# Optimization experiments

Measured on AMD Instinct MI355X. Metric: run time of the kernel, lower is better.

Reference implementation:

```python
import jax, jax.numpy as jnp
import numpy as np

N, DEG = 20000, 16
E = N * DEG
D_IN, D_HID, D_OUT, L = 1024, 512, 128, 3


def setup_inputs() -> dict:
    key = jax.random.key(0)
    ks = jax.random.split(key, 16)
    scale = 0.02
    X = jax.random.normal(ks[0], (N, D_IN), dtype=jnp.float32)
    senders = jax.random.randint(ks[1], (E,), 0, N)
    receivers = jnp.repeat(jnp.arange(N), DEG)  # sorted, every node has DEG neighbors
    inp = {"X": X, "senders": senders, "receivers": receivers}
    ki = 2
    for l in range(L):
        din = D_IN >> l
        dh = D_HID >> l
        inp[f"lw{l}"] = jax.random.normal(ks[ki], (2 * din, dh), jnp.float32) * scale; ki += 1
        inp[f"lb{l}"] = jnp.zeros((dh,), jnp.float32)
        inp[f"aw{l}"] = jax.random.normal(ks[ki], (din, dh), jnp.float32) * scale; ki += 1
        inp[f"aq{l}"] = jax.random.normal(ks[ki], (dh,), jnp.float32) * scale; ki += 1
    inp["ow"] = jax.random.normal(ks[ki], (D_HID >> (L - 1), D_OUT), jnp.float32) * scale
    inp["ob"] = jnp.zeros((D_OUT,), jnp.float32)
    return inp


def _attend(h, senders, receivers, aw, aq):
    # scores depend only on the neighbor (sender) embedding: q @ relu(W h_j)
    logits = jnp.einsum('nh,h->n', jax.nn.relu(h @ aw), aq)            # [N]
    el = logits[senders]                                               # [E]
    m = jax.ops.segment_max(el, receivers, num_segments=N)            # per-receiver max
    w = jnp.exp(el - m[receivers])                                     # [E]
    denom = jax.ops.segment_sum(w, receivers, num_segments=N)         # [N]
    msg = jax.ops.segment_sum(w[:, None] * h[senders], receivers, num_segments=N)  # [N,D]
    return msg / denom[:, None]


def reference(X, senders, receivers,
              lw0, lb0, aw0, aq0,
              lw1, lb1, aw1, aq1,
              lw2, lb2, aw2, aq2,
              ow, ob):
    params = [(lw0, lb0, aw0, aq0), (lw1, lb1, aw1, aq1), (lw2, lb2, aw2, aq2)]
    h = X
    for lw, lb, aw, aq in params:
        hN = _attend(h, senders, receivers, aw, aq)
        h = jax.nn.relu(jnp.concatenate([h, hN], axis=1) @ lw + lb)
    return h[14] @ ow + ob
```

## Files before the change

### kernel.cpp

```cpp
#include <hip/hip_runtime.h>
#include <math.h>

typedef unsigned short ushort_t;
typedef __attribute__((ext_vector_type(8))) short short8;
typedef __attribute__((ext_vector_type(4))) float f32x4;

#define NN    20000
#define DEG   16
constexpr int MAXL2 = 1 + DEG;
constexpr int MAXL1 = MAXL2 + MAXL2*DEG;
constexpr int MAXL0 = MAXL1*DEG;
constexpr int L0PAD = 73 * 64;
constexpr int NWBLK = 512;

__device__ __forceinline__ ushort_t f2bf(float f) {
    unsigned u = __float_as_uint(f);
    return (ushort_t)((u + 0x7FFFu + ((u >> 16) & 1u)) >> 16);
}

__global__ __launch_bounds__(256)
void k_frontier(const int* __restrict__ senders,
                int* list2, int* inv2, int* list1, int* inv1,
                int* list0, int* inv0, int* list3, int* cnts, float4* zp, int n4) {
    int t = threadIdx.x;
    if (blockIdx.x > 0) {
        int i = (blockIdx.x - 1) * 256 + t;
        if (i < n4) zp[i] = make_float4(0.f, 0.f, 0.f, 0.f);
        return;
    }
    __shared__ unsigned bm[625];
    __shared__ int cnt;
    auto clear = [&]() { for (int i = t; i < 625; i += 256) bm[i] = 0u; if (t == 0) cnt = 0; };
    auto tryadd = [&](int node, int* list, int* inv) {
        unsigned bit = 1u << (node & 31);
        unsigned old = atomicOr(&bm[node >> 5], bit);
        if (!(old & bit)) { int p = atomicAdd(&cnt, 1); list[p] = node; inv[node] = p; }
    };
    clear(); __syncthreads();
    if (t < 17) { int node = (t < 16) ? senders[14 * DEG + t] : 14; tryadd(node, list2, inv2); }
    __syncthreads();
    int c2 = cnt; if (t == 0) cnts[2] = c2;
    __syncthreads(); clear(); __syncthreads();
    for (int i = t; i < c2 * 17; i += 256) {
        int r = i / 17, k = i - 17 * r;
        int node = (k < 16) ? senders[list2[r] * DEG + k] : list2[r];
        tryadd(node, list1, inv1);
    }
    __syncthreads();
    int c1 = cnt; if (t == 0) cnts[1] = c1;
    __syncthreads(); clear(); __syncthreads();
    for (int i = t; i < c1 * 16; i += 256) {
        int r = i >> 4, k = i & 15;
        tryadd(senders[list1[r] * DEG + k], list0, inv0);
    }
    __syncthreads();
    if (t == 0) { cnts[0] = cnt; cnts[3] = 1; list3[0] = 14; }
}

__global__ __launch_bounds__(256)
void k_prep(const float* __restrict__ W, ushort_t* __restrict__ WT,
            const float* __restrict__ X, const int* __restrict__ list0,
            const int* __restrict__ cnt0, ushort_t* __restrict__ Xg) {
    int t = threadIdx.x;
    if (blockIdx.x < NWBLK) {
        __shared__ float tile[32][33];
        int b = blockIdx.x;
        int bx = b & 15, by = b >> 4;
        int i0 = t >> 3, j0 = (t & 7) * 4;
        int k = by * 32 + i0, n0 = bx * 32;
        float4 v = *(const float4*)(W + (size_t)k * 512 + n0 + j0);
        tile[i0][j0] = v.x; tile[i0][j0 + 1] = v.y; tile[i0][j0 + 2] = v.z; tile[i0][j0 + 3] = v.w;
        __syncthreads();
        int n = n0 + i0, kc = j0;
        ushort_t* p = WT + (size_t)n * 1024 + by * 32 + kc;
        p[0] = f2bf(tile[kc][i0]); p[1] = f2bf(tile[kc + 1][i0]);
        p[2] = f2bf(tile[kc + 2][i0]); p[3] = f2bf(tile[kc + 3][i0]);
    } else {
        int r = blockIdx.x - NWBLK;
        int rc = *cnt0;
        ushort_t o0 = 0, o1 = 0, o2 = 0, o3 = 0;
        if (r < rc) {
            float4 v = *(const float4*)(X + (size_t)list0[r] * 1024 + t * 4);
            o0 = f2bf(v.x); o1 = f2bf(v.y); o2 = f2bf(v.z); o3 = f2bf(v.w);
        }
        ushort_t* p = Xg + (size_t)r * 1024 + t * 4;
        p[0] = o0; p[1] = o1; p[2] = o2; p[3] = o3;
    }
}

__global__ __launch_bounds__(256)
void k_logits_mfma(const ushort_t* __restrict__ Xg,
                   const ushort_t* __restrict__ WT,
                   const float* __restrict__ aq, float* __restrict__ lgc,
                   const int* __restrict__ cnt, int K) {
    __shared__ short As[64 * 40];
    __shared__ short Bs[64 * 40];
    int rcnt = *cnt;
    int row0 = blockIdx.x * 64;
    if (row0 >= rcnt) return;
    int col0 = blockIdx.y * 64;
    int t = threadIdx.x;
    int w = t >> 6, lane = t & 63;

    int sr = t >> 2, sk = (t & 3) * 8;
    const ushort_t* ap = Xg + (size_t)(row0 + sr) * K + sk;
    const ushort_t* bp = WT + (size_t)(col0 + sr) * K + sk;

    int fm = lane & 15, fq = lane >> 4;
    const short* arow = As + (w * 16 + fm) * 40 + fq * 8;
    const short* brow = Bs + fm * 40 + fq * 8;

    f32x4 acc0 = {0.f,0.f,0.f,0.f}, acc1 = {0.f,0.f,0.f,0.f};
    f32x4 acc2 = {0.f,0.f,0.f,0.f}, acc3 = {0.f,0.f,0.f,0.f};

    short8 pa = *(const short8*)(ap);
    short8 pb = *(const short8*)(bp);
    for (int k0 = 0; k0 < K; k0 += 32) {
        *(short8*)(As + sr * 40 + sk) = pa;
        *(short8*)(Bs + sr * 40 + sk) = pb;
        __syncthreads();
        if (k0 + 32 < K) {
            pa = *(const short8*)(ap + k0 + 32);
            pb = *(const short8*)(bp + k0 + 32);
        }
        short8 af = *(const short8*)arow;
        short8 b0 = *(const short8*)(brow);
        short8 b1 = *(const short8*)(brow + 16 * 40);
        short8 b2 = *(const short8*)(brow + 32 * 40);
        short8 b3 = *(const short8*)(brow + 48 * 40);
        acc0 = __builtin_amdgcn_mfma_f32_16x16x32_bf16(af, b0, acc0, 0, 0, 0);
        acc1 = __builtin_amdgcn_mfma_f32_16x16x32_bf16(af, b1, acc1, 0, 0, 0);
        acc2 = __builtin_amdgcn_mfma_f32_16x16x32_bf16(af, b2, acc2, 0, 0, 0);
        acc3 = __builtin_amdgcn_mfma_f32_16x16x32_bf16(af, b3, acc3, 0, 0, 0);
        __syncthreads();
    }

    float aqv0 = aq[col0 + fm], aqv1 = aq[col0 + 16 + fm];
    float aqv2 = aq[col0 + 32 + fm], aqv3 = aq[col0 + 48 + fm];
#pragma unroll
    for (int r = 0; r < 4; r++) {
        float v = fmaxf(acc0[r], 0.f) * aqv0 + fmaxf(acc1[r], 0.f) * aqv1
                + fmaxf(acc2[r], 0.f) * aqv2 + fmaxf(acc3[r], 0.f) * aqv3;
#pragma unroll
        for (int off = 1; off < 16; off <<= 1) v += __shfl_xor(v, off);
        if (fm == 0) atomicAdd(&lgc[row0 + w * 16 + fq * 4 + r], v);
    }
}

__global__ __launch_bounds__(256)
void k_matmul(const float* __restrict__ A1, const float* __restrict__ A2,
              const int* __restrict__ list, const int* __restrict__ inv,
              const float* __restrict__ B, const float* __restrict__ aq,
              float* __restrict__ C, const int* __restrict__ cnt,
              int amode, int omode, int K1, int K2, int NC, int KS) {
    __shared__ float As[32][68];
    __shared__ float Bs[32][64];
    __shared__ float rowsum[64];

    int rcnt = *cnt;
    int row0 = blockIdx.x * 64;
    if (row0 >= rcnt) return;
    int col0 = blockIdx.y * 64;
    int K = K1 + K2;
    int kbeg = blockIdx.z * KS;
    int kend = kbeg + KS; if (kend > K) kend = K;

    int t = threadIdx.x;
    int ty = t >> 4, tx = t & 15;
    int lr = t >> 2, kaoff = (t & 3) * 4;
    int grow = row0 + lr;
    bool rowValid = grow < rcnt;
    const float* rp1 = A1;
    const float* rp2 = A2;
    if (rowValid) {
        int hrow;
        if (amode == 0) hrow = grow;
        else { int node = list[grow]; hrow = (amode == 2) ? inv[node] : node; }
        rp1 = A1 + (size_t)hrow * K1;
        rp2 = A2 + (size_t)grow * K2;
    }
    const float* Bp = B + col0;
    int bidx0 = t, bidx1 = t + 256;

    auto loadA = [&](int k) -> float4 {
        if (!rowValid) return make_float4(0.f, 0.f, 0.f, 0.f);
        const float* src = (k < K1) ? (rp1 + k) : (rp2 + (k - K1));
        return *(const float4*)src;
    };
    auto loadB = [&](int idx, int k0) -> float4 {
        int row = idx >> 4, c4 = (idx & 15) * 4;
        return *(const float4*)(Bp + (size_t)(k0 + row) * NC + c4);
    };

    float4 pa0 = loadA(kbeg + kaoff);
    float4 pa1 = loadA(kbeg + kaoff + 16);
    float4 pb0 = loadB(bidx0, kbeg);
    float4 pb1 = loadB(bidx1, kbeg);

    float acc[4][4] = {};
    for (int k0 = kbeg; k0 < kend; k0 += 32) {
        As[kaoff + 0][lr] = pa0.x; As[kaoff + 1][lr] = pa0.y;
        As[kaoff + 2][lr] = pa0.z; As[kaoff + 3][lr] = pa0.w;
        As[kaoff + 16][lr] = pa1.x; As[kaoff + 17][lr] = pa1.y;
        As[kaoff + 18][lr] = pa1.z; As[kaoff + 19][lr] = pa1.w;
        *(float4*)&Bs[bidx0 >> 4][(bidx0 & 15) * 4] = pb0;
        *(float4*)&Bs[bidx1 >> 4][(bidx1 & 15) * 4] = pb1;
        __syncthreads();
        if (k0 + 32 < kend) {
            pa0 = loadA(k0 + 32 + kaoff);
            pa1 = loadA(k0 + 32 + kaoff + 16);
            pb0 = loadB(bidx0, k0 + 32);
            pb1 = loadB(bidx1, k0 + 32);
        }
#pragma unroll
        for (int kk = 0; kk < 32; kk++) {
            float4 a4 = *(const float4*)&As[kk][ty * 4];
            float4 b4 = *(const float4*)&Bs[kk][tx * 4];
            float a[4] = {a4.x, a4.y, a4.z, a4.w};
            float b[4] = {b4.x, b4.y, b4.z, b4.w};
#pragma unroll
            for (int i = 0; i < 4; i++)
#pragma unroll
                for (int j = 0; j < 4; j++) acc[i][j] += a[i] * b[j];
        }
        __syncthreads();
    }

    if (omode == 0) {
#pragma unroll
        for (int i = 0; i < 4; i++) {
            int r = row0 + ty * 4 + i;
            if (r < rcnt) {
                float* Crow = C + (size_t)r * NC + col0 + tx * 4;
#pragma unroll
                for (int j = 0; j < 4; j++) atomicAdd(&Crow[j], acc[i][j]);
            }
        }
    } else {
        if (t < 64) rowsum[t] = 0.f;
        __syncthreads();
        float aqv[4];
#pragma unroll
        for (int j = 0; j < 4; j++) aqv[j] = aq[col0 + tx * 4 + j];
#pragma unroll
        for (int i = 0; i < 4; i++) {
            float s = 0.f;
#pragma unroll
            for (int j = 0; j < 4; j++) {
                float v = acc[i][j];
                v = v > 0.f ? v : 0.f;
                s += v * aqv[j];
            }
            atomicAdd(&rowsum[ty * 4 + i], s);
        }
        __syncthreads();
        if (t < 64) {
            int r = row0 + t;
            if (r < rcnt) atomicAdd(&C[r], rowsum[t]);
        }
    }
}

__global__ void k_bias_relu(const float* __restrict__ C, const float* __restrict__ b,
                            float* __restrict__ H, const int* __restrict__ cnt, int ncShift) {
    int rcnt = *cnt;
    int NC = 1 << ncShift;
    int e = blockIdx.x * 256 + threadIdx.x;
    int r = e >> ncShift;
    if (r >= rcnt) return;
    int c = e & (NC - 1);
    float v = C[(size_t)r * NC + c] + b[c];
    H[(size_t)r * NC + c] = v > 0.f ? v : 0.f;
}

__global__ __launch_bounds__(256)
void k_agg(const float* __restrict__ Hsrc, const int* __restrict__ invH,
           const float* __restrict__ lgc, const int* __restrict__ invL,
           const int* __restrict__ senders,
           const int* __restrict__ listN, const int* __restrict__ cntN,
           float* __restrict__ hN, int din) {
    __shared__ int   s_row[DEG];
    __shared__ float s_w[DEG];
    __shared__ float s_scale;
    int b = blockIdx.x;
    if (b >= *cntN) return;
    int n = listN[b];
    int t = threadIdx.x;
    if (t < DEG) {
        int s = senders[n * DEG + t];
        s_row[t] = invH ? invH[s] : s;
        s_w[t] = lgc[invL ? invL[s] : s];
    }
    __syncthreads();
    if (t == 0) {
        float m = -1e30f;
        for (int k = 0; k < DEG; k++) m = fmaxf(m, s_w[k]);
        float d = 0.f;
        for (int k = 0; k < DEG; k++) { float w = expf(s_w[k] - m); s_w[k] = w; d += w; }
        s_scale = 1.f / d;
    }
    __syncthreads();
    float scale = s_scale;
    for (int dI = t; dI < din; dI += 256) {
        float acc = 0.f;
#pragma unroll
        for (int k = 0; k < DEG; k++)
            acc += s_w[k] * Hsrc[(size_t)s_row[k] * din + dI];
        hN[(size_t)b * din + dI] = acc * scale;
    }
}

__global__ __launch_bounds__(512)
void k_out(const float* __restrict__ C2, const float* __restrict__ lb2,
           const float* __restrict__ OW, const float* __restrict__ OB,
           float* __restrict__ out) {
    __shared__ float h3s[128];
    __shared__ float part[4][128];
    int t = threadIdx.x;
    if (t < 128) { float v = C2[t] + lb2[t]; h3s[t] = v > 0.f ? v : 0.f; }
    __syncthreads();
    int j = t & 127, s = t >> 7;
    float a = 0.f;
    for (int k = s * 32; k < s * 32 + 32; k++) a += h3s[k] * OW[(size_t)k * 128 + j];
    part[s][j] = a;
    __syncthreads();
    if (t < 128) out[t] = OB[t] + part[0][t] + part[1][t] + part[2][t] + part[3][t];
}

extern "C" void kernel_launch(void* const* d_in, const int* in_sizes, int n_in,
                              void* d_out, int out_size, void* d_ws, size_t ws_size,
                              hipStream_t stream) {
    const float* X       = (const float*)d_in[0];
    const int*   senders = (const int*)d_in[1];
    const float* lw0 = (const float*)d_in[3];
    const float* lb0 = (const float*)d_in[4];
    const float* aw0 = (const float*)d_in[5];
    const float* aq0 = (const float*)d_in[6];
    const float* lw1 = (const float*)d_in[7];
    const float* lb1 = (const float*)d_in[8];
    const float* aw1 = (const float*)d_in[9];
    const float* aq1 = (const float*)d_in[10];
    const float* lw2 = (const float*)d_in[11];
    const float* lb2 = (const float*)d_in[12];
    const float* aw2 = (const float*)d_in[13];
    const float* aq2 = (const float*)d_in[14];
    const float* owp = (const float*)d_in[15];
    const float* obp = (const float*)d_in[16];
    float* out = (float*)d_out;

    char* ws = (char*)d_ws;
    size_t off = 0;
    auto alloc = [&](size_t nbytes) -> void* {
        void* p = ws + off;
        off += (nbytes + 255) & ~(size_t)255;
        return p;
    };
    float* lgc0 = (float*)alloc(L0PAD * 4);
    float* lgc1 = (float*)alloc(MAXL1 * 4);
    float* lgc2 = (float*)alloc(MAXL2 * 4);
    float* C0   = (float*)alloc((size_t)MAXL1 * 512 * 4);
    float* C1   = (float*)alloc((size_t)MAXL2 * 256 * 4);
    float* C2   = (float*)alloc(128 * 4);
    size_t zero_end = off;
    int* inv0  = (int*)alloc(NN * 4);
    int* inv1  = (int*)alloc(NN * 4);
    int* inv2  = (int*)alloc(NN * 4);
    int* list0 = (int*)alloc(L0PAD * 4);
    int* list1 = (int*)alloc(MAXL1 * 4);
    int* list2 = (int*)alloc(MAXL2 * 4);
    int* list3 = (int*)alloc(4);
    int* cnts  = (int*)alloc(4 * 4);
    ushort_t* Xg  = (ushort_t*)alloc((size_t)L0PAD * 1024 * 2);
    ushort_t* awT = (ushort_t*)alloc((size_t)512 * 1024 * 2);
    float* hN0c = (float*)alloc((size_t)MAXL1 * 1024 * 4);
    float* h1c  = (float*)alloc((size_t)MAXL1 * 512 * 4);
    float* hN1c = (float*)alloc((size_t)MAXL2 * 512 * 4);
    float* h2c  = (float*)alloc((size_t)MAXL2 * 256 * 4);
    float* hN2c = (float*)alloc(256 * 4);
    (void)in_sizes; (void)n_in; (void)out_size; (void)ws_size;

    int nz4 = (int)(zero_end / 16);
    int nzb = (nz4 + 255) / 256;

    hipLaunchKernelGGL(k_frontier, dim3(1 + nzb), dim3(256), 0, stream,
                       senders, list2, inv2, list1, inv1, list0, inv0, list3, cnts,
                       (float4*)ws, nz4);
    hipLaunchKernelGGL(k_prep, dim3(NWBLK + L0PAD), dim3(256), 0, stream,
                       aw0, awT, X, list0, cnts + 0, Xg);

    hipLaunchKernelGGL(k_logits_mfma, dim3(73, 512 / 64, 1), dim3(256), 0, stream,
                       Xg, awT, aq0, lgc0, cnts + 0, 1024);
    hipLaunchKernelGGL(k_agg, dim3(MAXL1), dim3(256), 0, stream,
                       X, (const int*)nullptr, lgc0, inv0, senders, list1, cnts + 1, hN0c, 1024);
    hipLaunchKernelGGL(k_matmul, dim3((MAXL1 + 63) / 64, 512 / 64, 8), dim3(256), 0, stream,
                       X, hN0c, list1, (int*)nullptr, lw0, aq0, C0, cnts + 1,
                       1, 0, 1024, 1024, 512, 256);
    hipLaunchKernelGGL(k_bias_relu, dim3((MAXL1 * 512 + 255) / 256), dim3(256), 0, stream,
                       C0, lb0, h1c, cnts + 1, 9);

    hipLaunchKernelGGL(k_matmul, dim3((MAXL1 + 63) / 64, 256 / 64, 1), dim3(256), 0, stream,
                       h1c, h1c, list1, (int*)nullptr, aw1, aq1, lgc1, cnts + 1,
                       0, 1, 512, 0, 256, 512);
    hipLaunchKernelGGL(k_agg, dim3(MAXL2), dim3(256), 0, stream,
                       h1c, inv1, lgc1, inv1, senders, list2, cnts + 2, hN1c, 512);
    hipLaunchKernelGGL(k_matmul, dim3(1, 256 / 64, 8), dim3(256), 0, stream,
                       h1c, hN1c, list2, inv1, lw1, aq1, C1, cnts + 2,
                       2, 0, 512, 512, 256, 128);
    hipLaunchKernelGGL(k_bias_relu, dim3((MAXL2 * 256 + 255) / 256), dim3(256), 0, stream,
                       C1, lb1, h2c, cnts + 2, 8);

    hipLaunchKernelGGL(k_matmul, dim3(1, 128 / 64, 1), dim3(256), 0, stream,
                       h2c, h2c, list2, (int*)nullptr, aw2, aq2, lgc2, cnts + 2,
                       0, 1, 256, 0, 128, 256);
    hipLaunchKernelGGL(k_agg, dim3(1), dim3(256), 0, stream,
                       h2c, inv2, lgc2, inv2, senders, list3, cnts + 3, hN2c, 256);
    hipLaunchKernelGGL(k_matmul, dim3(1, 128 / 64, 4), dim3(256), 0, stream,
                       h2c, hN2c, list3, inv2, lw2, aq2, C2, cnts + 3,
                       2, 0, 256, 256, 128, 128);
    hipLaunchKernelGGL(k_out, dim3(1), dim3(512), 0, stream, C2, lb2, owp, obp, out);
}
```

Baseline: 284.1 us.

## Fuse all GNN stages into one persistent kernel with grid-wide barriers

Replaces roughly a dozen separate kernel launches with a single persistent kernel of 256 blocks. The stages are separated by software grid barriers built on global atomic counters. It also drops the level-0 frontier dedup: each edge's sender row is gathered straight into the bf16 staging buffer, and attention logits are indexed per edge. The workspace is zeroed with a memset instead of extra zeroing blocks. This removes launch overhead and inter-kernel gaps, but adds spin-barrier cost and relies on all 256 blocks being co-resident. It also computes duplicate logits for repeated senders.

```diff
diff --git a/kernel.cpp b/kernel.cpp
--- a/kernel.cpp
+++ b/kernel.cpp
@@ -9,163 +9,34 @@
 #define DEG   16
 constexpr int MAXL2 = 1 + DEG;
 constexpr int MAXL1 = MAXL2 + MAXL2*DEG;
-constexpr int MAXL0 = MAXL1*DEG;
 constexpr int L0PAD = 73 * 64;
-constexpr int NWBLK = 512;
+constexpr int GRID  = 256;
 
 __device__ __forceinline__ ushort_t f2bf(float f) {
     unsigned u = __float_as_uint(f);
     return (ushort_t)((u + 0x7FFFu + ((u >> 16) & 1u)) >> 16);
 }
-
-__global__ __launch_bounds__(256)
-void k_frontier(const int* __restrict__ senders,
-                int* list2, int* inv2, int* list1, int* inv1,
-                int* list0, int* inv0, int* list3, int* cnts, float4* zp, int n4) {
-    int t = threadIdx.x;
-    if (blockIdx.x > 0) {
-        int i = (blockIdx.x - 1) * 256 + t;
-        if (i < n4) zp[i] = make_float4(0.f, 0.f, 0.f, 0.f);
-        return;
-    }
-    __shared__ unsigned bm[625];
-    __shared__ int cnt;
-    auto clear = [&]() { for (int i = t; i < 625; i += 256) bm[i] = 0u; if (t == 0) cnt = 0; };
-    auto tryadd = [&](int node, int* list, int* inv) {
-        unsigned bit = 1u << (node & 31);
-        unsigned old = atomicOr(&bm[node >> 5], bit);
-        if (!(old & bit)) { int p = atomicAdd(&cnt, 1); list[p] = node; inv[node] = p; }
-    };
-    clear(); __syncthreads();
-    if (t < 17) { int node = (t < 16) ? senders[14 * DEG + t] : 14; tryadd(node, list2, inv2); }
+__device__ __forceinline__ int ldacq(int* p) { return atomicAdd(p, 0); }
+
+struct WS {
+    int* bars;
+    float *lgc0, *lgc1, *lgc2;
+    float *C0, *C1, *C2;
+    int *inv1, *inv2, *list1, *list2, *list3, *cnts;
+    ushort_t *Xg, *awT;
+    float *hN0c, *h1c, *hN1c, *h2c, *hN2c;
+};
+
+__device__ void dev_mm(char* smem, int t,
+                       const float* A1, const float* A2, const int* list, const int* inv,
+                       const float* B, const float* aq, float* C, int rcnt,
+                       int amode, int omode, int K1, int K2, int NC,
+                       int row0, int col0, int kbeg, int kend) {
+    float* As = (float*)smem;
+    float* Bs = As + 32 * 68;
+    float* rowsum = (float*)(smem + 16896);
     __syncthreads();
-    int c2 = cnt; if (t == 0) cnts[2] = c2;
-    __syncthreads(); clear(); __syncthreads();
-    for (int i = t; i < c2 * 17; i += 256) {
-        int r = i / 17, k = i - 17 * r;
-        int node = (k < 16) ? senders[list2[r] * DEG + k] : list2[r];
-        tryadd(node, list1, inv1);
-    }
-    __syncthreads();
-    int c1 = cnt; if (t == 0) cnts[1] = c1;
-    __syncthreads(); clear(); __syncthreads();
-    for (int i = t; i < c1 * 16; i += 256) {
-        int r = i >> 4, k = i & 15;
-        tryadd(senders[list1[r] * DEG + k], list0, inv0);
-    }
-    __syncthreads();
-    if (t == 0) { cnts[0] = cnt; cnts[3] = 1; list3[0] = 14; }
-}
-
-__global__ __launch_bounds__(256)
-void k_prep(const float* __restrict__ W, ushort_t* __restrict__ WT,
-            const float* __restrict__ X, const int* __restrict__ list0,
-            const int* __restrict__ cnt0, ushort_t* __restrict__ Xg) {
-    int t = threadIdx.x;
-    if (blockIdx.x < NWBLK) {
-        __shared__ float tile[32][33];
-        int b = blockIdx.x;
-        int bx = b & 15, by = b >> 4;
-        int i0 = t >> 3, j0 = (t & 7) * 4;
-        int k = by * 32 + i0, n0 = bx * 32;
-        float4 v = *(const float4*)(W + (size_t)k * 512 + n0 + j0);
-        tile[i0][j0] = v.x; tile[i0][j0 + 1] = v.y; tile[i0][j0 + 2] = v.z; tile[i0][j0 + 3] = v.w;
-        __syncthreads();
-        int n = n0 + i0, kc = j0;
-        ushort_t* p = WT + (size_t)n * 1024 + by * 32 + kc;
-        p[0] = f2bf(tile[kc][i0]); p[1] = f2bf(tile[kc + 1][i0]);
-        p[2] = f2bf(tile[kc + 2][i0]); p[3] = f2bf(tile[kc + 3][i0]);
-    } else {
-        int r = blockIdx.x - NWBLK;
-        int rc = *cnt0;
-        ushort_t o0 = 0, o1 = 0, o2 = 0, o3 = 0;
-        if (r < rc) {
-            float4 v = *(const float4*)(X + (size_t)list0[r] * 1024 + t * 4);
-            o0 = f2bf(v.x); o1 = f2bf(v.y); o2 = f2bf(v.z); o3 = f2bf(v.w);
-        }
-        ushort_t* p = Xg + (size_t)r * 1024 + t * 4;
-        p[0] = o0; p[1] = o1; p[2] = o2; p[3] = o3;
-    }
-}
-
-__global__ __launch_bounds__(256)
-void k_logits_mfma(const ushort_t* __restrict__ Xg,
-                   const ushort_t* __restrict__ WT,
-                   const float* __restrict__ aq, float* __restrict__ lgc,
-                   const int* __restrict__ cnt, int K) {
-    __shared__ short As[64 * 40];
-    __shared__ short Bs[64 * 40];
-    int rcnt = *cnt;
-    int row0 = blockIdx.x * 64;
-    if (row0 >= rcnt) return;
-    int col0 = blockIdx.y * 64;
-    int t = threadIdx.x;
-    int w = t >> 6, lane = t & 63;
-
-    int sr = t >> 2, sk = (t & 3) * 8;
-    const ushort_t* ap = Xg + (size_t)(row0 + sr) * K + sk;
-    const ushort_t* bp = WT + (size_t)(col0 + sr) * K + sk;
-
-    int fm = lane & 15, fq = lane >> 4;
-    const short* arow = As + (w * 16 + fm) * 40 + fq * 8;
-    const short* brow = Bs + fm * 40 + fq * 8;
-
-    f32x4 acc0 = {0.f,0.f,0.f,0.f}, acc1 = {0.f,0.f,0.f,0.f};
-    f32x4 acc2 = {0.f,0.f,0.f,0.f}, acc3 = {0.f,0.f,0.f,0.f};
-
-    short8 pa = *(const short8*)(ap);
-    short8 pb = *(const short8*)(bp);
-    for (int k0 = 0; k0 < K; k0 += 32) {
-        *(short8*)(As + sr * 40 + sk) = pa;
-        *(short8*)(Bs + sr * 40 + sk) = pb;
-        __syncthreads();
-        if (k0 + 32 < K) {
-            pa = *(const short8*)(ap + k0 + 32);
-            pb = *(const short8*)(bp + k0 + 32);
-        }
-        short8 af = *(const short8*)arow;
-        short8 b0 = *(const short8*)(brow);
-        short8 b1 = *(const short8*)(brow + 16 * 40);
-        short8 b2 = *(const short8*)(brow + 32 * 40);
-        short8 b3 = *(const short8*)(brow + 48 * 40);
-        acc0 = __builtin_amdgcn_mfma_f32_16x16x32_bf16(af, b0, acc0, 0, 0, 0);
-        acc1 = __builtin_amdgcn_mfma_f32_16x16x32_bf16(af, b1, acc1, 0, 0, 0);
-        acc2 = __builtin_amdgcn_mfma_f32_16x16x32_bf16(af, b2, acc2, 0, 0, 0);
-        acc3 = __builtin_amdgcn_mfma_f32_16x16x32_bf16(af, b3, acc3, 0, 0, 0);
-        __syncthreads();
-    }
-
-    float aqv0 = aq[col0 + fm], aqv1 = aq[col0 + 16 + fm];
-    float aqv2 = aq[col0 + 32 + fm], aqv3 = aq[col0 + 48 + fm];
-#pragma unroll
-    for (int r = 0; r < 4; r++) {
-        float v = fmaxf(acc0[r], 0.f) * aqv0 + fmaxf(acc1[r], 0.f) * aqv1
-                + fmaxf(acc2[r], 0.f) * aqv2 + fmaxf(acc3[r], 0.f) * aqv3;
-#pragma unroll
-        for (int off = 1; off < 16; off <<= 1) v += __shfl_xor(v, off);
-        if (fm == 0) atomicAdd(&lgc[row0 + w * 16 + fq * 4 + r], v);
-    }
-}
-
-__global__ __launch_bounds__(256)
-void k_matmul(const float* __restrict__ A1, const float* __restrict__ A2,
-              const int* __restrict__ list, const int* __restrict__ inv,
-              const float* __restrict__ B, const float* __restrict__ aq,
-              float* __restrict__ C, const int* __restrict__ cnt,
-              int amode, int omode, int K1, int K2, int NC, int KS) {
-    __shared__ float As[32][68];
-    __shared__ float Bs[32][64];
-    __shared__ float rowsum[64];
-
-    int rcnt = *cnt;
-    int row0 = blockIdx.x * 64;
-    if (row0 >= rcnt) return;
-    int col0 = blockIdx.y * 64;
-    int K = K1 + K2;
-    int kbeg = blockIdx.z * KS;
-    int kend = kbeg + KS; if (kend > K) kend = K;
-
-    int t = threadIdx.x;
+
     int ty = t >> 4, tx = t & 15;
     int lr = t >> 2, kaoff = (t & 3) * 4;
     int grow = row0 + lr;
@@ -199,12 +70,12 @@
 
     float acc[4][4] = {};
     for (int k0 = kbeg; k0 < kend; k0 += 32) {
-        As[kaoff + 0][lr] = pa0.x; As[kaoff + 1][lr] = pa0.y;
-        As[kaoff + 2][lr] = pa0.z; As[kaoff + 3][lr] = pa0.w;
-        As[kaoff + 16][lr] = pa1.x; As[kaoff + 17][lr] = pa1.y;
-        As[kaoff + 18][lr] = pa1.z; As[kaoff + 19][lr] = pa1.w;
-        *(float4*)&Bs[bidx0 >> 4][(bidx0 & 15) * 4] = pb0;
-        *(float4*)&Bs[bidx1 >> 4][(bidx1 & 15) * 4] = pb1;
+        As[(kaoff + 0) * 68 + lr] = pa0.x; As[(kaoff + 1) * 68 + lr] = pa0.y;
+        As[(kaoff + 2) * 68 + lr] = pa0.z; As[(kaoff + 3) * 68 + lr] = pa0.w;
+        As[(kaoff + 16) * 68 + lr] = pa1.x; As[(kaoff + 17) * 68 + lr] = pa1.y;
+        As[(kaoff + 18) * 68 + lr] = pa1.z; As[(kaoff + 19) * 68 + lr] = pa1.w;
+        *(float4*)&Bs[(bidx0 >> 4) * 64 + (bidx0 & 15) * 4] = pb0;
+        *(float4*)&Bs[(bidx1 >> 4) * 64 + (bidx1 & 15) * 4] = pb1;
         __syncthreads();
         if (k0 + 32 < kend) {
             pa0 = loadA(k0 + 32 + kaoff);
@@ -214,8 +85,8 @@
         }
 #pragma unroll
         for (int kk = 0; kk < 32; kk++) {
-            float4 a4 = *(const float4*)&As[kk][ty * 4];
-            float4 b4 = *(const float4*)&Bs[kk][tx * 4];
+            float4 a4 = *(const float4*)&As[kk * 68 + ty * 4];
+            float4 b4 = *(const float4*)&Bs[kk * 64 + tx * 4];
             float a[4] = {a4.x, a4.y, a4.z, a4.w};
             float b[4] = {b4.x, b4.y, b4.z, b4.w};
 #pragma unroll
@@ -261,70 +132,251 @@
     }
 }
 
-__global__ void k_bias_relu(const float* __restrict__ C, const float* __restrict__ b,
-                            float* __restrict__ H, const int* __restrict__ cnt, int ncShift) {
-    int rcnt = *cnt;
-    int NC = 1 << ncShift;
-    int e = blockIdx.x * 256 + threadIdx.x;
-    int r = e >> ncShift;
-    if (r >= rcnt) return;
-    int c = e & (NC - 1);
-    float v = C[(size_t)r * NC + c] + b[c];
-    H[(size_t)r * NC + c] = v > 0.f ? v : 0.f;
-}
-
-__global__ __launch_bounds__(256)
-void k_agg(const float* __restrict__ Hsrc, const int* __restrict__ invH,
-           const float* __restrict__ lgc, const int* __restrict__ invL,
-           const int* __restrict__ senders,
-           const int* __restrict__ listN, const int* __restrict__ cntN,
-           float* __restrict__ hN, int din) {
-    __shared__ int   s_row[DEG];
-    __shared__ float s_w[DEG];
-    __shared__ float s_scale;
-    int b = blockIdx.x;
-    if (b >= *cntN) return;
-    int n = listN[b];
-    int t = threadIdx.x;
+__device__ void dev_logits_mfma(char* smem, int t,
+                                const ushort_t* Xg, const ushort_t* WT,
+                                const float* aq, float* lgc,
+                                int row0, int col0, int K) {
+    short* As = (short*)smem;
+    short* Bs = As + 64 * 40;
+    __syncthreads();
+    int w = t >> 6, lane = t & 63;
+    int sr = t >> 2, sk = (t & 3) * 8;
+    const ushort_t* ap = Xg + (size_t)(row0 + sr) * K + sk;
+    const ushort_t* bp = WT + (size_t)(col0 + sr) * K + sk;
+    int fm = lane & 15, fq = lane >> 4;
+    const short* arow = As + (w * 16 + fm) * 40 + fq * 8;
+    const short* brow = Bs + fm * 40 + fq * 8;
+
+    f32x4 acc0 = {0.f,0.f,0.f,0.f}, acc1 = {0.f,0.f,0.f,0.f};
+    f32x4 acc2 = {0.f,0.f,0.f,0.f}, acc3 = {0.f,0.f,0.f,0.f};
+
+    short8 pa = *(const short8*)(ap);
+    short8 pb = *(const short8*)(bp);
+    for (int k0 = 0; k0 < K; k0 += 32) {
+        *(short8*)(As + sr * 40 + sk) = pa;
+        *(short8*)(Bs + sr * 40 + sk) = pb;
+        __syncthreads();
+        if (k0 + 32 < K) {
+            pa = *(const short8*)(ap + k0 + 32);
+            pb = *(const short8*)(bp + k0 + 32);
+        }
+        short8 af = *(const short8*)arow;
+        short8 b0 = *(const short8*)(brow);
+        short8 b1 = *(const short8*)(brow + 16 * 40);
+        short8 b2 = *(const short8*)(brow + 32 * 40);
+        short8 b3 = *(const short8*)(brow + 48 * 40);
+        acc0 = __builtin_amdgcn_mfma_f32_16x16x32_bf16(af, b0, acc0, 0, 0, 0);
+        acc1 = __builtin_amdgcn_mfma_f32_16x16x32_bf16(af, b1, acc1, 0, 0, 0);
+        acc2 = __builtin_amdgcn_mfma_f32_16x16x32_bf16(af, b2, acc2, 0, 0, 0);
+        acc3 = __builtin_amdgcn_mfma_f32_16x16x32_bf16(af, b3, acc3, 0, 0, 0);
+        __syncthreads();
+    }
+    float aqv0 = aq[col0 + fm], aqv1 = aq[col0 + 16 + fm];
+    float aqv2 = aq[col0 + 32 + fm], aqv3 = aq[col0 + 48 + fm];
+#pragma unroll
+    for (int r = 0; r < 4; r++) {
+        float v = fmaxf(acc0[r], 0.f) * aqv0 + fmaxf(acc1[r], 0.f) * aqv1
+                + fmaxf(acc2[r], 0.f) * aqv2 + fmaxf(acc3[r], 0.f) * aqv3;
+#pragma unroll
+        for (int off = 1; off < 16; off <<= 1) v += __shfl_xor(v, off);
+        if (fm == 0) atomicAdd(&lgc[row0 + w * 16 + fq * 4 + r], v);
+    }
+}
+
+__device__ void dev_agg(int t, const int* senders_row, const int* inv,
+                        const float* lgc, int edgeBase,
+                        const float* Hsrc, int din, float* outp,
+                        int* s_row, float* s_w, float* s_scale) {
+    __syncthreads();
     if (t < DEG) {
-        int s = senders[n * DEG + t];
-        s_row[t] = invH ? invH[s] : s;
-        s_w[t] = lgc[invL ? invL[s] : s];
+        int s = senders_row[t];
+        int rr = inv ? inv[s] : s;
+        s_row[t] = rr;
+        s_w[t] = (edgeBase >= 0) ? lgc[edgeBase + t] : lgc[rr];
     }
     __syncthreads();
     if (t == 0) {
         float m = -1e30f;
         for (int k = 0; k < DEG; k++) m = fmaxf(m, s_w[k]);
         float d = 0.f;
-        for (int k = 0; k < DEG; k++) { float w = expf(s_w[k] - m); s_w[k] = w; d += w; }
-        s_scale = 1.f / d;
+        for (int k = 0; k < DEG; k++) { float v = expf(s_w[k] - m); s_w[k] = v; d += v; }
+        *s_scale = 1.f / d;
     }
     __syncthreads();
-    float scale = s_scale;
-    for (int dI = t; dI < din; dI += 256) {
-        float acc = 0.f;
-#pragma unroll
-        for (int k = 0; k < DEG; k++)
-            acc += s_w[k] * Hsrc[(size_t)s_row[k] * din + dI];
-        hN[(size_t)b * din + dI] = acc * scale;
-    }
-}
-
-__global__ __launch_bounds__(512)
-void k_out(const float* __restrict__ C2, const float* __restrict__ lb2,
-           const float* __restrict__ OW, const float* __restrict__ OB,
-           float* __restrict__ out) {
-    __shared__ float h3s[128];
-    __shared__ float part[4][128];
-    int t = threadIdx.x;
-    if (t < 128) { float v = C2[t] + lb2[t]; h3s[t] = v > 0.f ? v : 0.f; }
-    __syncthreads();
-    int j = t & 127, s = t >> 7;
-    float a = 0.f;
-    for (int k = s * 32; k < s * 32 + 32; k++) a += h3s[k] * OW[(size_t)k * 128 + j];
-    part[s][j] = a;
-    __syncthreads();
-    if (t < 128) out[t] = OB[t] + part[0][t] + part[1][t] + part[2][t] + part[3][t];
+    float sc = *s_scale;
+    for (int c = t; c < din; c += 256) {
+        float a = 0.f;
+#pragma unroll
+        for (int k = 0; k < DEG; k++) a += s_w[k] * Hsrc[(size_t)s_row[k] * din + c];
+        outp[c] = a * sc;
+    }
+}
+
+__global__ __launch_bounds__(256, 2)
+void k_mega(const float* __restrict__ X, const int* __restrict__ senders,
+            const float* lw0, const float* lb0, const float* aw0, const float* aq0,
+            const float* lw1, const float* lb1, const float* aw1, const float* aq1,
+            const float* lw2, const float* lb2, const float* aw2, const float* aq2,
+            const float* ow, const float* ob, float* out, WS w) {
+    __shared__ char smem[17408];
+    __shared__ int   s_row[DEG];
+    __shared__ float s_w[DEG];
+    __shared__ float s_scale;
+    __shared__ int   fcnt;
+    int t = threadIdx.x, bid = blockIdx.x;
+
+    auto gsync = [&](int idx) {
+        __syncthreads();
+        if (t == 0) {
+            __threadfence();
+            atomicAdd(&w.bars[idx], 1);
+            while (atomicAdd(&w.bars[idx], 0) < GRID) __builtin_amdgcn_s_sleep(2);
+            __threadfence();
+        }
+        __syncthreads();
+    };
+
+    if (bid == 0) {
+        unsigned* bm = (unsigned*)smem;
+        for (int i = t; i < 625; i += 256) bm[i] = 0u;
+        if (t == 0) fcnt = 0;
+        __syncthreads();
+        if (t < 17) {
+            int node = (t < 16) ? senders[14 * DEG + t] : 14;
+            unsigned bit = 1u << (node & 31);
+            if (!(atomicOr(&bm[node >> 5], bit) & bit)) {
+                int p = atomicAdd(&fcnt, 1); w.list2[p] = node; w.inv2[node] = p;
+            }
+        }
+        __syncthreads();
+        int c2 = fcnt;
+        __syncthreads();
+        for (int i = t; i < 625; i += 256) bm[i] = 0u;
+        if (t == 0) { w.cnts[2] = c2; fcnt = 0; }
+        __syncthreads();
+        for (int i = t; i < c2 * 17; i += 256) {
+            int r = i / 17, k = i - 17 * r;
+            int node = (k < 16) ? senders[w.list2[r] * DEG + k] : w.list2[r];
+            unsigned bit = 1u << (node & 31);
+            if (!(atomicOr(&bm[node >> 5], bit) & bit)) {
+                int p = atomicAdd(&fcnt, 1); w.list1[p] = node; w.inv1[node] = p;
+            }
+        }
+        __syncthreads();
+        if (t == 0) { w.cnts[1] = fcnt; w.cnts[3] = 1; w.list3[0] = 14; }
+    } else {
+        float* tile = (float*)smem;
+        for (int b = bid - 1; b < 512; b += GRID - 1) {
+            __syncthreads();
+            int bx = b & 15, by = b >> 4;
+            int i0 = t >> 3, j0 = (t & 7) * 4;
+            float4 v = *(const float4*)(aw0 + (size_t)(by * 32 + i0) * 512 + bx * 32 + j0);
+            tile[i0 * 33 + j0] = v.x; tile[i0 * 33 + j0 + 1] = v.y;
+            tile[i0 * 33 + j0 + 2] = v.z; tile[i0 * 33 + j0 + 3] = v.w;
+            __syncthreads();
+            ushort_t* p = w.awT + (size_t)(bx * 32 + i0) * 1024 + by * 32 + j0;
+            p[0] = f2bf(tile[(j0 + 0) * 33 + i0]); p[1] = f2bf(tile[(j0 + 1) * 33 + i0]);
+            p[2] = f2bf(tile[(j0 + 2) * 33 + i0]); p[3] = f2bf(tile[(j0 + 3) * 33 + i0]);
+        }
+    }
+    gsync(0);
+
+    int rc1 = ldacq(&w.cnts[1]);
+    int rc2 = ldacq(&w.cnts[2]);
+    int ne = rc1 * DEG;
+
+    for (int e = bid; e < L0PAD; e += GRID) {
+        unsigned lo = 0, hi = 0;
+        if (e < ne) {
+            int node = senders[w.list1[e >> 4] * DEG + (e & 15)];
+            float4 v = *(const float4*)(X + (size_t)node * 1024 + t * 4);
+            lo = (unsigned)f2bf(v.x) | ((unsigned)f2bf(v.y) << 16);
+            hi = (unsigned)f2bf(v.z) | ((unsigned)f2bf(v.w) << 16);
+        }
+        *(uint2*)(w.Xg + (size_t)e * 1024 + t * 4) = make_uint2(lo, hi);
+    }
+    gsync(1);
+
+    for (int task = bid; task < 73 * 8; task += GRID) {
+        int xr = task % 73, yc = task / 73;
+        dev_logits_mfma(smem, t, w.Xg, w.awT, aq0, w.lgc0, xr * 64, yc * 64, 1024);
+    }
+    gsync(2);
+
+    for (int r = bid; r < rc1; r += GRID)
+        dev_agg(t, senders + (size_t)w.list1[r] * DEG, nullptr, w.lgc0, r * DEG,
+                X, 1024, w.hN0c + (size_t)r * 1024, s_row, s_w, &s_scale);
+    gsync(3);
+
+    for (int task = bid; task < 5 * 8 * 8; task += GRID) {
+        int z = task / 40, rem = task % 40, x = rem % 5, y = rem / 5;
+        if (x * 64 < rc1)
+            dev_mm(smem, t, X, w.hN0c, w.list1, nullptr, lw0, aq0, w.C0, rc1,
+                   1, 0, 1024, 1024, 512, x * 64, y * 64, z * 256, z * 256 + 256);
+    }
+    gsync(4);
+
+    for (int i = bid * 256 + t; i < rc1 * 512; i += GRID * 256) {
+        float v = w.C0[i] + lb0[i & 511];
+        w.h1c[i] = v > 0.f ? v : 0.f;
+    }
+    gsync(5);
+
+    for (int task = bid; task < 5 * 4; task += GRID) {
+        int x = task % 5, y = task / 5;
+        if (x * 64 < rc1)
+            dev_mm(smem, t, w.h1c, w.h1c, nullptr, nullptr, aw1, aq1, w.lgc1, rc1,
+                   0, 1, 512, 0, 256, x * 64, y * 64, 0, 512);
+    }
+    gsync(6);
+
+    for (int r = bid; r < rc2; r += GRID)
+        dev_agg(t, senders + (size_t)w.list2[r] * DEG, w.inv1, w.lgc1, -1,
+                w.h1c, 512, w.hN1c + (size_t)r * 512, s_row, s_w, &s_scale);
+    gsync(7);
+
+    for (int task = bid; task < 4 * 8; task += GRID) {
+        int y = task & 3, z = task >> 2;
+        dev_mm(smem, t, w.h1c, w.hN1c, w.list2, w.inv1, lw1, aq1, w.C1, rc2,
+               2, 0, 512, 512, 256, 0, y * 64, z * 128, z * 128 + 128);
+    }
+    gsync(8);
+
+    for (int i = bid * 256 + t; i < rc2 * 256; i += GRID * 256) {
+        float v = w.C1[i] + lb1[i & 255];
+        w.h2c[i] = v > 0.f ? v : 0.f;
+    }
+    gsync(9);
+
+    for (int task = bid; task < 2; task += GRID)
+        dev_mm(smem, t, w.h2c, w.h2c, nullptr, nullptr, aw2, aq2, w.lgc2, rc2,
+               0, 1, 256, 0, 128, 0, task * 64, 0, 256);
+    gsync(10);
+
+    if (bid == 0)
+        dev_agg(t, senders + 14 * DEG, w.inv2, w.lgc2, -1,
+                w.h2c, 256, w.hN2c, s_row, s_w, &s_scale);
+    gsync(11);
+
+    for (int task = bid; task < 2 * 4; task += GRID) {
+        int y = task & 1, z = task >> 1;
+        dev_mm(smem, t, w.h2c, w.hN2c, w.list3, w.inv2, lw2, aq2, w.C2, 1,
+               2, 0, 256, 256, 128, 0, y * 64, z * 128, z * 128 + 128);
+    }
+    gsync(12);
+
+    if (bid == 0) {
+        float* h3s = (float*)smem;
+        float* part = h3s + 128;
+        if (t < 128) { float v = w.C2[t] + lb2[t]; h3s[t] = v > 0.f ? v : 0.f; }
+        __syncthreads();
+        int j = t & 127, s = t >> 7;
+        float a = 0.f;
+        for (int k = s * 64; k < s * 64 + 64; k++) a += h3s[k] * ow[(size_t)k * 128 + j];
+        part[s * 128 + j] = a;
+        __syncthreads();
+        if (t < 128) out[t] = ob[t] + part[t] + part[128 + t];
+    }
 }
 
 extern "C" void kernel_launch(void* const* d_in, const int* in_sizes, int n_in,
@@ -355,67 +407,32 @@
         off += (nbytes + 255) & ~(size_t)255;
         return p;
     };
-    float* lgc0 = (float*)alloc(L0PAD * 4);
-    float* lgc1 = (float*)alloc(MAXL1 * 4);
-    float* lgc2 = (float*)alloc(MAXL2 * 4);
-    float* C0   = (float*)alloc((size_t)MAXL1 * 512 * 4);
-    float* C1   = (float*)alloc((size_t)MAXL2 * 256 * 4);
-    float* C2   = (float*)alloc(128 * 4);
+    WS w;
+    w.bars = (int*)alloc(64 * 4);
+    w.lgc0 = (float*)alloc(L0PAD * 4);
+    w.lgc1 = (float*)alloc(MAXL1 * 4);
+    w.lgc2 = (float*)alloc(MAXL2 * 4);
+    w.C0   = (float*)alloc((size_t)MAXL1 * 512 * 4);
+    w.C1   = (float*)alloc((size_t)MAXL2 * 256 * 4);
+    w.C2   = (float*)alloc(128 * 4);
     size_t zero_end = off;
-    int* inv0  = (int*)alloc(NN * 4);
-    int* inv1  = (int*)alloc(NN * 4);
-    int* inv2  = (int*)alloc(NN * 4);
-    int* list0 = (int*)alloc(L0PAD * 4);
-    int* list1 = (int*)alloc(MAXL1 * 4);
-    int* list2 = (int*)alloc(MAXL2 * 4);
-    int* list3 = (int*)alloc(4);
-    int* cnts  = (int*)alloc(4 * 4);
-    ushort_t* Xg  = (ushort_t*)alloc((size_t)L0PAD * 1024 * 2);
-    ushort_t* awT = (ushort_t*)alloc((size_t)512 * 1024 * 2);
-    float* hN0c = (float*)alloc((size_t)MAXL1 * 1024 * 4);
-    float* h1c  = (float*)alloc((size_t)MAXL1 * 512 * 4);
-    float* hN1c = (float*)alloc((size_t)MAXL2 * 512 * 4);
-    float* h2c  = (float*)alloc((size_t)MAXL2 * 256 * 4);
-    float* hN2c = (float*)alloc(256 * 4);
+    w.inv1  = (int*)alloc(NN * 4);
+    w.inv2  = (int*)alloc(NN * 4);
+    w.list1 = (int*)alloc(MAXL1 * 4);
+    w.list2 = (int*)alloc(MAXL2 * 4);
+    w.list3 = (int*)alloc(4);
+    w.cnts  = (int*)alloc(16);
+    w.Xg    = (ushort_t*)alloc((size_t)L0PAD * 1024 * 2);
+    w.awT   = (ushort_t*)alloc((size_t)512 * 1024 * 2);
+    w.hN0c  = (float*)alloc((size_t)MAXL1 * 1024 * 4);
+    w.h1c   = (float*)alloc((size_t)MAXL1 * 512 * 4);
+    w.hN1c  = (float*)alloc((size_t)MAXL2 * 512 * 4);
+    w.h2c   = (float*)alloc((size_t)MAXL2 * 256 * 4);
+    w.hN2c  = (float*)alloc(256 * 4);
     (void)in_sizes; (void)n_in; (void)out_size; (void)ws_size;
 
-    int nz4 = (int)(zero_end / 16);
-    int nzb = (nz4 + 255) / 256;
-
-    hipLaunchKernelGGL(k_frontier, dim3(1 + nzb), dim3(256), 0, stream,
-                       senders, list2, inv2, list1, inv1, list0, inv0, list3, cnts,
-                       (float4*)ws, nz4);
-    hipLaunchKernelGGL(k_prep, dim3(NWBLK + L0PAD), dim3(256), 0, stream,
-                       aw0, awT, X, list0, cnts + 0, Xg);
-
-    hipLaunchKernelGGL(k_logits_mfma, dim3(73, 512 / 64, 1), dim3(256), 0, stream,
-                       Xg, awT, aq0, lgc0, cnts + 0, 1024);
-    hipLaunchKernelGGL(k_agg, dim3(MAXL1), dim3(256), 0, stream,
-                       X, (const int*)nullptr, lgc0, inv0, senders, list1, cnts + 1, hN0c, 1024);
-    hipLaunchKernelGGL(k_matmul, dim3((MAXL1 + 63) / 64, 512 / 64, 8), dim3(256), 0, stream,
-                       X, hN0c, list1, (int*)nullptr, lw0, aq0, C0, cnts + 1,
-                       1, 0, 1024, 1024, 512, 256);
-    hipLaunchKernelGGL(k_bias_relu, dim3((MAXL1 * 512 + 255) / 256), dim3(256), 0, stream,
-                       C0, lb0, h1c, cnts + 1, 9);
-
-    hipLaunchKernelGGL(k_matmul, dim3((MAXL1 + 63) / 64, 256 / 64, 1), dim3(256), 0, stream,
-                       h1c, h1c, list1, (int*)nullptr, aw1, aq1, lgc1, cnts + 1,
-                       0, 1, 512, 0, 256, 512);
-    hipLaunchKernelGGL(k_agg, dim3(MAXL2), dim3(256), 0, stream,
-                       h1c, inv1, lgc1, inv1, senders, list2, cnts + 2, hN1c, 512);
-    hipLaunchKernelGGL(k_matmul, dim3(1, 256 / 64, 8), dim3(256), 0, stream,
-                       h1c, hN1c, list2, inv1, lw1, aq1, C1, cnts + 2,
-                       2, 0, 512, 512, 256, 128);
-    hipLaunchKernelGGL(k_bias_relu, dim3((MAXL2 * 256 + 255) / 256), dim3(256), 0, stream,
-                       C1, lb1, h2c, cnts + 2, 8);
-
-    hipLaunchKernelGGL(k_matmul, dim3(1, 128 / 64, 1), dim3(256), 0, stream,
-                       h2c, h2c, list2, (int*)nullptr, aw2, aq2, lgc2, cnts + 2,
-                       0, 1, 256, 0, 128, 256);
-    hipLaunchKernelGGL(k_agg, dim3(1), dim3(256), 0, stream,
-                       h2c, inv2, lgc2, inv2, senders, list3, cnts + 3, hN2c, 256);
-    hipLaunchKernelGGL(k_matmul, dim3(1, 128 / 64, 4), dim3(256), 0, stream,
-                       h2c, hN2c, list3, inv2, lw2, aq2, C2, cnts + 3,
-                       2, 0, 256, 256, 128, 128);
-    hipLaunchKernelGGL(k_out, dim3(1), dim3(512), 0, stream, C2, lb2, owp, obp, out);
-}
+    hipMemsetAsync(ws, 0, zero_end, stream);
+    hipLaunchKernelGGL(k_mega, dim3(GRID), dim3(256), 0, stream,
+                       X, senders, lw0, lb0, aw0, aq0, lw1, lb1, aw1, aq1,
+                       lw2, lb2, aw2, aq2, owp, obp, out, w);
+}
```

Result: slower. 492.6 us (+73.4%).
